# Kernel tuning notes

Measured on AMD Instinct MI355X. Metric: run time of the kernel, lower is better.

## Reference

```python
import jax, jax.numpy as jnp
import numpy as np

B, T, D = 2, 2048, 1024
H, KVH, HD = 16, 4, 64  # query heads, kv heads, head_dim
GROUPS = H // KVH


def apply_rope(x, cos, sin):
    # x: (B, nh, T, hd); cos/sin: (max_T, hd//2)
    t = x.shape[2]
    c = cos[:t][None, None]  # (1,1,T,hd//2)
    s = sin[:t][None, None]
    half = x.shape[-1] // 2
    x1, x2 = x[..., :half], x[..., half:]
    rotated = jnp.concatenate((-x2, x1), axis=-1)
    cf = jnp.concatenate((c, c), axis=-1)  # repeat(1,1,1,2)
    sf = jnp.concatenate((s, s), axis=-1)
    return x * cf + rotated * sf


def setup_inputs():
    key = jax.random.key(0)
    ks = jax.random.split(key, 5)
    x = jax.random.normal(ks[0], (B, T, D), dtype=jnp.float32)
    # RoPE tables: theta^(-i/half) frequencies
    half = HD // 2
    inv_freq = 1.0 / (10000.0 ** (jnp.arange(half, dtype=jnp.float32) / half))
    ang = jnp.arange(T, dtype=jnp.float32)[:, None] * inv_freq[None, :]  # (T, half)
    rope_cos = jnp.cos(ang)
    rope_sin = jnp.sin(ang)
    # Causal additive mask
    causal = jnp.tril(jnp.ones((T, T), dtype=bool))
    attention_mask = jnp.where(causal, 0.0, -1e9).astype(jnp.float32)[None, None]
    scale = 0.02
    Wq = jax.random.normal(ks[1], (D, D), dtype=jnp.float32) * scale
    Wk = jax.random.normal(ks[2], (D, KVH * HD), dtype=jnp.float32) * scale
    Wv = jax.random.normal(ks[3], (D, KVH * HD), dtype=jnp.float32) * scale
    Wo = jax.random.normal(ks[4], (D, D), dtype=jnp.float32) * scale
    return {"x": x, "rope_cos": rope_cos, "rope_sin": rope_sin,
            "attention_mask": attention_mask,
            "Wq": Wq, "Wk": Wk, "Wv": Wv, "Wo": Wo}


def reference(x, rope_cos, rope_sin, attention_mask, Wq, Wk, Wv, Wo):
    b, t, _ = x.shape
    q = (x @ Wq).reshape(b, t, H, HD).transpose(0, 2, 1, 3)      # (B,H,T,hd)
    k = (x @ Wk).reshape(b, t, KVH, HD).transpose(0, 2, 1, 3)    # (B,KVH,T,hd)
    v = (x @ Wv).reshape(b, t, KVH, HD).transpose(0, 2, 1, 3)
    q = apply_rope(q, rope_cos, rope_sin)
    k = apply_rope(k, rope_cos, rope_sin)
    if GROUPS > 1:
        k = jnp.repeat(k, GROUPS, axis=1)  # repeat_interleave over heads
        v = jnp.repeat(v, GROUPS, axis=1)
    scale = 1.0 / np.sqrt(HD)
    attn = jnp.einsum('bhqd,bhkd->bhqk', q, k) * scale
    attn = attn + attention_mask
    attn = jax.nn.softmax(attn.astype(jnp.float32), axis=-1).astype(q.dtype)
    out = jnp.einsum('bhqk,bhkd->bhqd', attn, v)
    out = out.transpose(0, 2, 1, 3).reshape(b, t, D)
    return out @ Wo
```

## Files before the change

kernel.cpp:

```cpp
#include <hip/hip_runtime.h>

typedef __attribute__((ext_vector_type(8))) short short8;
typedef __attribute__((ext_vector_type(4))) short short4v;
typedef __attribute__((ext_vector_type(4))) float f32x4;
typedef __attribute__((ext_vector_type(16))) float f32x16;
typedef __attribute__((ext_vector_type(2))) unsigned uint2v;
typedef __attribute__((ext_vector_type(4))) unsigned uint4v;

#define T_ 2048
#define H_ 16
#define KVH_ 4
#define QSCALE 0.18033688011112042f
#define DEFER 8.0f

__device__ inline unsigned short f2bf(float f) {
    unsigned u = __builtin_bit_cast(unsigned, f);
    u += 0x7fff + ((u >> 16) & 1);
    return (unsigned short)(u >> 16);
}
__device__ inline float bf2f(unsigned short v) {
    unsigned u = ((unsigned)v) << 16;
    return __builtin_bit_cast(float, u);
}
__device__ inline unsigned pk2(float lo, float hi) {
    unsigned r;
    asm("v_cvt_pk_bf16_f32 %0, %1, %2" : "=v"(r) : "v"(lo), "v"(hi));
    return r;
}

__device__ inline void gl_lds16(const unsigned short* g, unsigned short* lds) {
    __builtin_amdgcn_global_load_lds(
        (const __attribute__((address_space(1))) unsigned int*)g,
        (__attribute__((address_space(3))) unsigned int*)lds, 16, 0, 0);
}

__global__ void cast_bf16(const float* __restrict__ in,
                          unsigned short* __restrict__ out, int n8) {
    int i = blockIdx.x * blockDim.x + threadIdx.x;
    if (i >= n8) return;
    float4 v0 = ((const float4*)in)[i * 2];
    float4 v1 = ((const float4*)in)[i * 2 + 1];
    short8 o;
    o[0] = f2bf(v0.x); o[1] = f2bf(v0.y); o[2] = f2bf(v0.z); o[3] = f2bf(v0.w);
    o[4] = f2bf(v1.x); o[5] = f2bf(v1.y); o[6] = f2bf(v1.z); o[7] = f2bf(v1.w);
    ((short8*)out)[i] = o;
}

__global__ __launch_bounds__(256) void transpose_cast(
        const float* __restrict__ W, unsigned short* __restrict__ out,
        int K, int N, int rowoff) {
    __shared__ unsigned short ts[64][66];
    const int bx = blockIdx.x, by = blockIdx.y, tid = threadIdx.x;
    #pragma unroll
    for (int s = 0; s < 16; ++s) {
        int idx = tid + s * 256;
        int kl = idx >> 6, nl = idx & 63;
        ts[kl][nl] = f2bf(W[(size_t)(by * 64 + kl) * N + bx * 64 + nl]);
    }
    __syncthreads();
    #pragma unroll
    for (int s = 0; s < 16; ++s) {
        int idx = tid + s * 256;
        int nl = idx >> 6, kl = idx & 63;
        out[(size_t)(rowoff + bx * 64 + nl) * K + by * 64 + kl] = ts[kl][nl];
    }
}

template <int MODE>
__global__ __launch_bounds__(256) void gemm_mfma(
        const unsigned short* __restrict__ A,
        const unsigned short* __restrict__ Bt,
        void* __restrict__ Cq, unsigned short* __restrict__ Ck,
        unsigned short* __restrict__ Cvt,
        const float* __restrict__ rc, const float* __restrict__ rs,
        int M, int N, int K) {
    __shared__ __align__(16) unsigned short As[128 * 32];
    __shared__ __align__(16) unsigned short Bs[64 * 32];
    const int tid = threadIdx.x;
    const int w = tid >> 6, l = tid & 63, lk = l & 15, lg = l >> 4;
    const int bx = blockIdx.x, by = blockIdx.y;

    const unsigned short* Arow = A + (size_t)by * 128 * K;
    const unsigned short* Brow = Bt + (size_t)bx * 64 * K;

    f32x4 acc[2][4];
    #pragma unroll
    for (int m = 0; m < 2; ++m)
        #pragma unroll
        for (int n = 0; n < 4; ++n) acc[m][n] = (f32x4){0, 0, 0, 0};

    for (int k0 = 0; k0 < K; k0 += 32) {
        #pragma unroll
        for (int p = 0; p < 2; ++p) {
            int cb = p * 256 + w * 64;
            int c = cb + l;
            int row = c >> 2, ko = (c & 3) * 8;
            gl_lds16(Arow + (size_t)row * K + k0 + ko, As + cb * 8);
        }
        {
            int c = w * 64 + l;
            int row = c >> 2, ko = (c & 3) * 8;
            gl_lds16(Brow + (size_t)row * K + k0 + ko, Bs + c * 8);
        }
        __syncthreads();
        short8 aF[2], bF[4];
        #pragma unroll
        for (int m = 0; m < 2; ++m)
            aF[m] = *(const short8*)&As[(w * 32 + m * 16 + lk) * 32 + lg * 8];
        #pragma unroll
        for (int n = 0; n < 4; ++n)
            bF[n] = *(const short8*)&Bs[(n * 16 + lk) * 32 + lg * 8];
        #pragma unroll
        for (int m = 0; m < 2; ++m)
            #pragma unroll
            for (int n = 0; n < 4; ++n)
                acc[m][n] = __builtin_amdgcn_mfma_f32_16x16x32_bf16(
                    aF[m], bF[n], acc[m][n], 0, 0, 0);
        __syncthreads();
    }

    const int rowbase = by * 128 + w * 32;
    if constexpr (MODE == 0) {
        float* C = (float*)Cq;
        #pragma unroll
        for (int m = 0; m < 2; ++m)
            #pragma unroll
            for (int r = 0; r < 4; ++r) {
                size_t ro = (size_t)(rowbase + m * 16 + lg * 4 + r) * N + bx * 64 + lk;
                #pragma unroll
                for (int n = 0; n < 4; ++n) C[ro + n * 16] = acc[m][n][r];
            }
    }
    if constexpr (MODE == 1) {
        const int colgrp = bx;
        if (colgrp < 16) {
            unsigned short* C = (unsigned short*)Cq;
            const int h = colgrp;
            #pragma unroll
            for (int m = 0; m < 2; ++m)
                #pragma unroll
                for (int r = 0; r < 4; ++r) {
                    int trow = rowbase + m * 16 + lg * 4 + r;
                    int b = trow >> 11, t = trow & (T_ - 1);
                    size_t ob = (((size_t)(b * 16 + h)) * T_ + t) * 64;
                    #pragma unroll
                    for (int n = 0; n < 2; ++n) {
                        int d = n * 16 + lk;
                        float cc = rc[t * 32 + d], ss = rs[t * 32 + d];
                        float x1 = acc[m][n][r], x2 = acc[m][n + 2][r];
                        C[ob + d]      = f2bf((x1 * cc - x2 * ss) * QSCALE);
                        C[ob + d + 32] = f2bf((x2 * cc + x1 * ss) * QSCALE);
                    }
                }
        } else if (colgrp < 20) {
            const int kvh = colgrp - 16;
            #pragma unroll
            for (int m = 0; m < 2; ++m)
                #pragma unroll
                for (int r = 0; r < 4; ++r) {
                    int trow = rowbase + m * 16 + lg * 4 + r;
                    int b = trow >> 11, t = trow & (T_ - 1);
                    size_t ob = (((size_t)(b * 4 + kvh)) * T_ + t) * 64;
                    #pragma unroll
                    for (int n = 0; n < 2; ++n) {
                        int d = n * 16 + lk;
                        float cc = rc[t * 32 + d], ss = rs[t * 32 + d];
                        float x1 = acc[m][n][r], x2 = acc[m][n + 2][r];
                        Ck[ob + d]      = f2bf(x1 * cc - x2 * ss);
                        Ck[ob + d + 32] = f2bf(x2 * cc + x1 * ss);
                    }
                }
        } else {
            const int kvh = colgrp - 20;
            #pragma unroll
            for (int m = 0; m < 2; ++m) {
                int trow0 = rowbase + m * 16 + lg * 4;
                int b = trow0 >> 11, t0 = trow0 & (T_ - 1);
                #pragma unroll
                for (int n = 0; n < 4; ++n) {
                    int d = n * 16 + lk;
                    short4v pk;
                    #pragma unroll
                    for (int r = 0; r < 4; ++r) pk[r] = f2bf(acc[m][n][r]);
                    *(short4v*)(Cvt + (((size_t)(b * 4 + kvh)) * 64 + d) * T_ + t0) = pk;
                }
            }
        }
    }
}

#define SWC(row, col) ((col) ^ (((row) & 7) << 3))
#define CROW(r, hi) (((r) & 3) + 8 * ((r) >> 2) + 4 * (hi))

__global__ __launch_bounds__(256) void attn_mfma(
        const unsigned short* __restrict__ Q,
        const unsigned short* __restrict__ K,
        const unsigned short* __restrict__ Vt,
        unsigned short* __restrict__ O,
        float* __restrict__ PM, float* __restrict__ PLp,
        unsigned short* __restrict__ PACC) {
    __shared__ __align__(16) unsigned short Ks[2][64 * 64];
    __shared__ __align__(16) unsigned short Vs[2][64 * 64];

    const int bid = blockIdx.x;
    int bh, qt, kt0, ktend, ck;
    bool direct;
    if (bid < 256) {
        bh = bid & 31; qt = 8 + (bid >> 5);
        kt0 = 0; ktend = 16; ck = 0; direct = false;
    } else if (bid < 512) {
        int j = bid - 256;
        bh = j & 31; qt = 7 - (j >> 5);
        kt0 = 0; ktend = 2 * qt + 2; ck = 0; direct = true;
    } else {
        int j = bid - 512;
        bh = j & 31; qt = 15 - (j >> 5);
        kt0 = 16; ktend = 2 * qt + 2; ck = 1; direct = false;
    }
    const int nkt = ktend - kt0;
    const int h = bh & 15, b = bh >> 4, kv = h >> 2;
    const int tid = threadIdx.x;
    const int w = tid >> 6, l = tid & 63;
    const int q32 = l & 31, hi = l >> 5;

    const unsigned short* Kb = K + ((size_t)(b * 4 + kv)) * T_ * 64;
    const unsigned short* Vb = Vt + ((size_t)(b * 4 + kv)) * 64 * T_;

    short8 qf[4];
    {
        const unsigned short* qp =
            Q + (((size_t)(b * 16 + h)) * T_ + qt * 128 + w * 32 + q32) * 64 + hi * 8;
        #pragma unroll
        for (int s = 0; s < 4; ++s) qf[s] = *(const short8*)(qp + 16 * s);
    }

    f32x16 o0, o1;
    #pragma unroll
    for (int i = 0; i < 16; ++i) { o0[i] = 0.f; o1[i] = 0.f; }
    float mloc = -1e38f, lsum = 0.f;

    const int sr = l >> 3, sg = l & 7;
    auto stage = [&](int buf, int kt) {
        #pragma unroll
        for (int p = 0; p < 2; ++p) {
            const int ch = w * 2 + p;
            const int row = ch * 8 + sr;
            const int gs = (sg ^ sr) * 8;
            gl_lds16(Kb + ((size_t)(kt * 64 + row)) * 64 + gs, &Ks[buf][ch * 512]);
            gl_lds16(Vb + (size_t)row * T_ + kt * 64 + gs,     &Vs[buf][ch * 512]);
        }
    };

    auto mk = [&](float e0, float e1, float e2, float e3,
                  float e4, float e5, float e6, float e7) -> short8 {
        unsigned a0 = pk2(e0, e1);
        unsigned b0 = pk2(e4, e5);
        uint2v r02 = __builtin_amdgcn_permlane32_swap(a0, b0, false, false);
        unsigned a1 = pk2(e2, e3);
        unsigned b1 = pk2(e6, e7);
        uint2v r13 = __builtin_amdgcn_permlane32_swap(a1, b1, false, false);
        uint4v u;
        u[0] = r02[0]; u[1] = r13[0]; u[2] = r02[1]; u[3] = r13[1];
        return __builtin_bit_cast(short8, u);
    };

    stage(0, kt0);
    for (int i = 0; i < nkt; ++i) {
        const int kt = kt0 + i;
        const int cur = i & 1;
        __syncthreads();
        if (i + 1 < nkt) stage(cur ^ 1, kt0 + i + 1);

        f32x16 st0, st1;
        #pragma unroll
        for (int r = 0; r < 16; ++r) { st0[r] = 0.f; st1[r] = 0.f; }
        __builtin_amdgcn_s_setprio(1);
        #pragma unroll
        for (int s = 0; s < 4; ++s) {
            const int c = 16 * s + hi * 8;
            const int kr0 = q32, kr1 = 32 + q32;
            short8 k0 = *(const short8*)&Ks[cur][kr0 * 64 + SWC(kr0, c)];
            short8 k1 = *(const short8*)&Ks[cur][kr1 * 64 + SWC(kr1, c)];
            st0 = __builtin_amdgcn_mfma_f32_32x32x16_bf16(k0, qf[s], st0, 0, 0, 0);
            st1 = __builtin_amdgcn_mfma_f32_32x32x16_bf16(k1, qf[s], st1, 0, 0, 0);
        }
        __builtin_amdgcn_s_setprio(0);

        if (kt >= 2 * qt) {
            const int qg = qt * 128 + w * 32 + q32;
            #pragma unroll
            for (int r = 0; r < 16; ++r) {
                const int kg = kt * 64 + CROW(r, hi);
                if (kg > qg)      st0[r] = -1e30f;
                if (kg + 32 > qg) st1[r] = -1e30f;
            }
        }

        float pm = st0[0];
        #pragma unroll
        for (int r = 1; r < 16; ++r) pm = fmaxf(pm, st0[r]);
        #pragma unroll
        for (int r = 0; r < 16; ++r) pm = fmaxf(pm, st1[r]);
        pm = fmaxf(pm, __shfl_xor(pm, 32));

        if (__any(pm > mloc + DEFER)) {
            const float nm = fmaxf(mloc, pm);
            const float corr = exp2f(mloc - nm);
            mloc = nm;
            lsum *= corr;
            #pragma unroll
            for (int r = 0; r < 16; ++r) {
                const float cr = __shfl(corr, CROW(r, hi));
                o0[r] *= cr;
                o1[r] *= cr;
            }
        }

        float ls = 0.f;
        #pragma unroll
        for (int r = 0; r < 16; ++r) {
            st0[r] = exp2f(st0[r] - mloc); ls += st0[r];
            st1[r] = exp2f(st1[r] - mloc); ls += st1[r];
        }
        ls += __shfl_xor(ls, 32);
        lsum += ls;

        short8 pa0 = mk(st0[0], st0[1], st0[2],  st0[3],  st0[4],  st0[5],  st0[6],  st0[7]);
        short8 pa1 = mk(st0[8], st0[9], st0[10], st0[11], st0[12], st0[13], st0[14], st0[15]);
        short8 pa2 = mk(st1[0], st1[1], st1[2],  st1[3],  st1[4],  st1[5],  st1[6],  st1[7]);
        short8 pa3 = mk(st1[8], st1[9], st1[10], st1[11], st1[12], st1[13], st1[14], st1[15]);

        __builtin_amdgcn_s_setprio(1);
        const int vd0 = q32, vd1 = 32 + q32;
        #pragma unroll
        for (int ks = 0; ks < 4; ++ks) {
            short8 paf = (ks == 0) ? pa0 : (ks == 1) ? pa1 : (ks == 2) ? pa2 : pa3;
            const int c = 16 * ks + hi * 8;
            short8 vb0 = *(const short8*)&Vs[cur][vd0 * 64 + SWC(vd0, c)];
            short8 vb1 = *(const short8*)&Vs[cur][vd1 * 64 + SWC(vd1, c)];
            o0 = __builtin_amdgcn_mfma_f32_32x32x16_bf16(paf, vb0, o0, 0, 0, 0);
            o1 = __builtin_amdgcn_mfma_f32_32x32x16_bf16(paf, vb1, o1, 0, 0, 0);
        }
        __builtin_amdgcn_s_setprio(0);
    }

    if (direct) {
        #pragma unroll
        for (int r = 0; r < 16; ++r) {
            const float inv = 1.f / __shfl(lsum, CROW(r, hi));
            const int t = qt * 128 + w * 32 + CROW(r, hi);
            unsigned short* op = &O[(((size_t)(b * T_ + t)) * 16 + h) * 64 + q32];
            op[0]  = f2bf(o0[r] * inv);
            op[32] = f2bf(o1[r] * inv);
        }
    } else {
        const int p = ((bh << 3) + (qt - 8)) * 2 + ck;
        if (l < 32) {
            PM[p * 128 + w * 32 + l]  = mloc;
            PLp[p * 128 + w * 32 + l] = lsum;
        }
        #pragma unroll
        for (int r = 0; r < 16; ++r) {
            const int row = w * 32 + CROW(r, hi);
            unsigned short* pp = &PACC[((size_t)p * 128 + row) * 64 + q32];
            pp[0]  = f2bf(o0[r]);
            pp[32] = f2bf(o1[r]);
        }
    }
}

__global__ __launch_bounds__(256) void combine_attn(
        const float* __restrict__ PM, const float* __restrict__ PLp,
        const unsigned short* __restrict__ PACC,
        unsigned short* __restrict__ O) {
    const int cid = blockIdx.x;
    const int bh = cid & 31, qt = 8 + (cid >> 5);
    const int h = bh & 15, b = bh >> 4;
    const int tid = threadIdx.x;
    const int row = tid >> 1, cg = (tid & 1) * 32;
    const int p0 = ((bh << 3) + (qt - 8)) * 2, p1 = p0 + 1;

    float mA = PM[p0 * 128 + row], mB = PM[p1 * 128 + row];
    float lA = PLp[p0 * 128 + row], lB = PLp[p1 * 128 + row];
    float M = fmaxf(mA, mB);
    float wA = exp2f(mA - M), wB = exp2f(mB - M);
    float inv = 1.f / (lA * wA + lB * wB);
    wA *= inv; wB *= inv;

    const unsigned short* a = &PACC[((size_t)p0 * 128 + row) * 64 + cg];
    const unsigned short* c = &PACC[((size_t)p1 * 128 + row) * 64 + cg];
    int t = qt * 128 + row;
    unsigned short* op = &O[(((size_t)(b * T_ + t)) * 16 + h) * 64 + cg];
    #pragma unroll
    for (int j = 0; j < 4; ++j) {
        short8 va = *(const short8*)(a + j * 8);
        short8 vb = *(const short8*)(c + j * 8);
        short8 o;
        #pragma unroll
        for (int i = 0; i < 8; ++i)
            o[i] = f2bf(bf2f((unsigned short)va[i]) * wA +
                        bf2f((unsigned short)vb[i]) * wB);
        *(short8*)(op + j * 8) = o;
    }
}

extern "C" void kernel_launch(void* const* d_in, const int* in_sizes, int n_in,
                              void* d_out, int out_size, void* d_ws, size_t ws_size,
                              hipStream_t stream) {
    const float* x  = (const float*)d_in[0];
    const float* rc = (const float*)d_in[1];
    const float* rs = (const float*)d_in[2];
    const float* Wq = (const float*)d_in[4];
    const float* Wk = (const float*)d_in[5];
    const float* Wv = (const float*)d_in[6];
    const float* Wo = (const float*)d_in[7];
    float* out = (float*)d_out;

    unsigned short* ws = (unsigned short*)d_ws;
    unsigned short* xb  = ws;
    unsigned short* Wt  = ws + 4194304;
    unsigned short* Wot = ws + 5767168;
    unsigned short* Qbf = ws + 6815744;
    unsigned short* Kbf = ws + 11010048;
    unsigned short* Vtb = ws + 12058624;
    unsigned short* Ob  = ws + 13107200;

    float* PM            = (float*)d_ws;
    float* PLp           = PM + 512 * 128;
    unsigned short* PACC = (unsigned short*)(PLp + 512 * 128);

    dim3 blk(256);
    cast_bf16<<<2048, blk, 0, stream>>>(x, xb, 524288);
    transpose_cast<<<dim3(16, 16), blk, 0, stream>>>(Wq, Wt, 1024, 1024, 0);
    transpose_cast<<<dim3(4, 16),  blk, 0, stream>>>(Wk, Wt, 1024, 256, 1024);
    transpose_cast<<<dim3(4, 16),  blk, 0, stream>>>(Wv, Wt, 1024, 256, 1280);
    transpose_cast<<<dim3(16, 16), blk, 0, stream>>>(Wo, Wot, 1024, 1024, 0);

    gemm_mfma<1><<<dim3(24, 32), blk, 0, stream>>>(
        xb, Wt, (void*)Qbf, Kbf, Vtb, rc, rs, 4096, 1536, 1024);

    attn_mfma<<<dim3(768), blk, 0, stream>>>(Qbf, Kbf, Vtb, Ob, PM, PLp, PACC);
    combine_attn<<<dim3(256), blk, 0, stream>>>(PM, PLp, PACC, Ob);

    gemm_mfma<0><<<dim3(16, 32), blk, 0, stream>>>(
        Ob, Wot, (void*)out, nullptr, nullptr, nullptr, nullptr, 4096, 1024, 1024);
}
```

Baseline: 120.0 us.

## Store K/V tiles in LDS in MFMA fragment order and tree-reduce softmax

The K and V staging into shared memory now writes each 16-byte chunk in the exact lane order the MFMA operand fragments need. Reads become contiguous per-lane loads at (chunk*64+lane)*8 with no XOR swizzle or address arithmetic. The row max and row sum also switch from linear serial chains to pairwise tree reductions, which shortens the dependency chain. The global loads lose their row-contiguous swizzled pattern and may coalesce less well, since each lane now fetches a 16-byte piece from a different row.

```diff
diff --git a/kernel.cpp b/kernel.cpp
--- a/kernel.cpp
+++ b/kernel.cpp
@@ -189,7 +189,6 @@
     }
 }
 
-#define SWC(row, col) ((col) ^ (((row) & 7) << 3))
 #define CROW(r, hi) (((r) & 3) + 8 * ((r) >> 2) + 4 * (hi))
 
 __global__ __launch_bounds__(256) void attn_mfma(
@@ -199,8 +198,8 @@
         unsigned short* __restrict__ O,
         float* __restrict__ PM, float* __restrict__ PLp,
         unsigned short* __restrict__ PACC) {
-    __shared__ __align__(16) unsigned short Ks[2][64 * 64];
-    __shared__ __align__(16) unsigned short Vs[2][64 * 64];
+    __shared__ __align__(16) unsigned short Ks[2][8 * 512];
+    __shared__ __align__(16) unsigned short Vs[2][8 * 512];
 
     const int bid = blockIdx.x;
     int bh, qt, kt0, ktend, ck;
@@ -239,15 +238,15 @@
     for (int i = 0; i < 16; ++i) { o0[i] = 0.f; o1[i] = 0.f; }
     float mloc = -1e38f, lsum = 0.f;
 
-    const int sr = l >> 3, sg = l & 7;
     auto stage = [&](int buf, int kt) {
         #pragma unroll
         for (int p = 0; p < 2; ++p) {
             const int ch = w * 2 + p;
-            const int row = ch * 8 + sr;
-            const int gs = (sg ^ sr) * 8;
-            gl_lds16(Kb + ((size_t)(kt * 64 + row)) * 64 + gs, &Ks[buf][ch * 512]);
-            gl_lds16(Vb + (size_t)row * T_ + kt * 64 + gs,     &Vs[buf][ch * 512]);
+            const int half = ch >> 2, sub = ch & 3;
+            gl_lds16(Kb + ((size_t)(kt * 64 + half * 32 + q32)) * 64 + 16 * sub + hi * 8,
+                     &Ks[buf][ch * 512]);
+            gl_lds16(Vb + ((size_t)(half * 32 + q32)) * T_ + kt * 64 + 16 * sub + hi * 8,
+                     &Vs[buf][ch * 512]);
         }
     };
 
@@ -277,10 +276,8 @@
         __builtin_amdgcn_s_setprio(1);
         #pragma unroll
         for (int s = 0; s < 4; ++s) {
-            const int c = 16 * s + hi * 8;
-            const int kr0 = q32, kr1 = 32 + q32;
-            short8 k0 = *(const short8*)&Ks[cur][kr0 * 64 + SWC(kr0, c)];
-            short8 k1 = *(const short8*)&Ks[cur][kr1 * 64 + SWC(kr1, c)];
+            short8 k0 = *(const short8*)&Ks[cur][(s * 64 + l) * 8];
+            short8 k1 = *(const short8*)&Ks[cur][((4 + s) * 64 + l) * 8];
             st0 = __builtin_amdgcn_mfma_f32_32x32x16_bf16(k0, qf[s], st0, 0, 0, 0);
             st1 = __builtin_amdgcn_mfma_f32_32x32x16_bf16(k1, qf[s], st1, 0, 0, 0);
         }
@@ -296,12 +293,14 @@
             }
         }
 
-        float pm = st0[0];
-        #pragma unroll
-        for (int r = 1; r < 16; ++r) pm = fmaxf(pm, st0[r]);
-        #pragma unroll
-        for (int r = 0; r < 16; ++r) pm = fmaxf(pm, st1[r]);
-        pm = fmaxf(pm, __shfl_xor(pm, 32));
+        float tm[16];
+        #pragma unroll
+        for (int r = 0; r < 16; ++r) tm[r] = fmaxf(st0[r], st1[r]);
+        #pragma unroll
+        for (int d = 8; d >= 1; d >>= 1)
+            #pragma unroll
+            for (int r = 0; r < d; ++r) tm[r] = fmaxf(tm[r], tm[r + d]);
+        float pm = fmaxf(tm[0], __shfl_xor(tm[0], 32));
 
         if (__any(pm > mloc + DEFER)) {
             const float nm = fmaxf(mloc, pm);
@@ -316,14 +315,18 @@
             }
         }
 
-        float ls = 0.f;
+        float ts[16];
         #pragma unroll
         for (int r = 0; r < 16; ++r) {
-            st0[r] = exp2f(st0[r] - mloc); ls += st0[r];
-            st1[r] = exp2f(st1[r] - mloc); ls += st1[r];
-        }
-        ls += __shfl_xor(ls, 32);
-        lsum += ls;
+            st0[r] = exp2f(st0[r] - mloc);
+            st1[r] = exp2f(st1[r] - mloc);
+            ts[r] = st0[r] + st1[r];
+        }
+        #pragma unroll
+        for (int d = 8; d >= 1; d >>= 1)
+            #pragma unroll
+            for (int r = 0; r < d; ++r) ts[r] += ts[r + d];
+        lsum += ts[0] + __shfl_xor(ts[0], 32);
 
         short8 pa0 = mk(st0[0], st0[1], st0[2],  st0[3],  st0[4],  st0[5],  st0[6],  st0[7]);
         short8 pa1 = mk(st0[8], st0[9], st0[10], st0[11], st0[12], st0[13], st0[14], st0[15]);
@@ -331,13 +334,11 @@
         short8 pa3 = mk(st1[8], st1[9], st1[10], st1[11], st1[12], st1[13], st1[14], st1[15]);
 
         __builtin_amdgcn_s_setprio(1);
-        const int vd0 = q32, vd1 = 32 + q32;
         #pragma unroll
         for (int ks = 0; ks < 4; ++ks) {
             short8 paf = (ks == 0) ? pa0 : (ks == 1) ? pa1 : (ks == 2) ? pa2 : pa3;
-            const int c = 16 * ks + hi * 8;
-            short8 vb0 = *(const short8*)&Vs[cur][vd0 * 64 + SWC(vd0, c)];
-            short8 vb1 = *(const short8*)&Vs[cur][vd1 * 64 + SWC(vd1, c)];
+            short8 vb0 = *(const short8*)&Vs[cur][(ks * 64 + l) * 8];
+            short8 vb1 = *(const short8*)&Vs[cur][((4 + ks) * 64 + l) * 8];
             o0 = __builtin_amdgcn_mfma_f32_32x32x16_bf16(paf, vb0, o0, 0, 0, 0);
             o1 = __builtin_amdgcn_mfma_f32_32x32x16_bf16(paf, vb1, o1, 0, 0, 0);
         }
```

After: 124.0 us. 1.03x slower.
